# Performance work log

Measured on AMD Instinct MI355X. Metric: run time of the kernel, lower is better.

Reference implementation:

```python
import jax, jax.numpy as jnp
import numpy as np

HIDDEN = 1024
NUM_HEADS = 16
HEAD_SIZE = HIDDEN // NUM_HEADS  # 64
SQ, SK, B = 256, 1024, 8


def setup_inputs() -> dict:
    key = jax.random.key(0)
    ks = jax.random.split(key, 8)
    s = 0.02
    return {
        "x": jax.random.normal(ks[0], (SQ, B, HIDDEN), jnp.float32),
        "memory": jax.random.normal(ks[1], (SK, B, HIDDEN), jnp.float32),
        "Wq": jax.random.normal(ks[2], (HIDDEN, HIDDEN), jnp.float32) * s,
        "bq": jax.random.normal(ks[3], (HIDDEN,), jnp.float32) * s,
        "Wkv": jax.random.normal(ks[4], (2 * HIDDEN, HIDDEN), jnp.float32) * s,
        "bkv": jax.random.normal(ks[5], (2 * HIDDEN,), jnp.float32) * s,
        "Wd": jax.random.normal(ks[6], (HIDDEN, HIDDEN), jnp.float32) * s,
        "bd": jax.random.normal(ks[7], (HIDDEN,), jnp.float32) * s,
    }


def reference(x, memory, Wq, bq, Wkv, bkv, Wd, bd):
    # x: (Sq, B, E), memory: (Sk, B, E)  -- sequence-first layout
    Sq, Bb, E = x.shape
    Sk = memory.shape[0]
    H, Dh = NUM_HEADS, HEAD_SIZE

    q = x @ Wq.T + bq            # (Sq, B, E)
    kv = memory @ Wkv.T + bkv    # (Sk, B, 2E)

    # view (..., H, Dh) then composite permute (1,3,0,2):
    # NOTE: the original module's chained permutes put tensors in
    # (batch, head_size, seq, num_heads) layout, so the score matmul
    # contracts over num_heads and head_size acts as the head axis.
    q = q.reshape(Sq, Bb, H, Dh).transpose((1, 3, 0, 2))          # (B, Dh, Sq, H)
    kv = kv.reshape(Sk, Bb, H, 2 * Dh)
    k = kv[..., :Dh].transpose((1, 3, 0, 2))                       # (B, Dh, Sk, H)
    v = kv[..., Dh:].transpose((1, 3, 0, 2))                       # (B, Dh, Sk, H)

    scale = 1.0 / np.sqrt(float(Dh)).astype(np.float32)
    scores = jnp.einsum('bdqh,bdkh->bdqk', q, k) * scale           # (B, Dh, Sq, Sk)
    attn = jax.nn.softmax(scores, axis=-1)
    # attention_dropout omitted (eval mode / p=0)
    ctx = jnp.einsum('bdqk,bdkh->bdqh', attn, v)                   # (B, Dh, Sq, H)

    # transpose(1,2) -> (B, Sq, Dh, H), reshape concatenates Dh-major
    ctx = ctx.transpose((0, 2, 1, 3)).reshape(Bb, Sq, E)
    ctx = ctx.transpose((1, 0, 2))                                 # (Sq, B, E)
    out = ctx @ Wd.T + bd
    # output dropout omitted (eval mode / p=0)
    return out
```

## Files before the change

### kernel.cpp

```cpp
#include <hip/hip_runtime.h>


typedef float f32x4 __attribute__((ext_vector_type(4)));
typedef __bf16 bf16x8 __attribute__((ext_vector_type(8)));
typedef short s16x8 __attribute__((ext_vector_type(8)));
typedef unsigned int u32x2 __attribute__((ext_vector_type(2)));

__device__ __forceinline__ unsigned short f2bf(float f) {
    unsigned int u = __builtin_bit_cast(unsigned int, f);
    u += 0x7fffu + ((u >> 16) & 1u);
    return (unsigned short)(u >> 16);
}
__device__ __forceinline__ unsigned cvt_pk_bf16(float lo, float hi_) {
    unsigned r;
    asm("v_cvt_pk_bf16_f32 %0, %1, %2" : "=v"(r) : "v"(lo), "v"(hi_));
    return r;
}

__global__ void cvt_f32_bf16(const float* __restrict__ src,
                             unsigned short* __restrict__ dst) {
    int i = (blockIdx.x * 256 + threadIdx.x) * 8;
    float4 a = *reinterpret_cast<const float4*>(src + i);
    float4 b = *reinterpret_cast<const float4*>(src + i + 4);
    s16x8 o;
    o[0] = (short)f2bf(a.x); o[1] = (short)f2bf(a.y);
    o[2] = (short)f2bf(a.z); o[3] = (short)f2bf(a.w);
    o[4] = (short)f2bf(b.x); o[5] = (short)f2bf(b.y);
    o[6] = (short)f2bf(b.z); o[7] = (short)f2bf(b.w);
    *reinterpret_cast<s16x8*>(dst + i) = o;
}

template <int OUT_BF16>
__global__ __launch_bounds__(256, 2)
void gemm_bt(const unsigned short* __restrict__ A,
             const unsigned short* __restrict__ Bw,
             const float* __restrict__ bias,
             void* __restrict__ Cout,
             int M, int N, int K, float scale) {
    __shared__ unsigned short As[128][64];
    __shared__ unsigned short Bs[128][64];

    const int tid = threadIdx.x;
    const int bm = blockIdx.x, bn = blockIdx.y;
    const int lane = tid & 63;
    const int w = tid >> 6;
    const int wr = w >> 1, wc = w & 1;
    const int l15 = lane & 15, lg = lane >> 4;

    f32x4 acc[4][4] = {};

    for (int k0 = 0; k0 < K; k0 += 64) {
#pragma unroll
        for (int it = 0; it < 8; ++it) {
            const int isB = it >> 2;
            int cc = ((it & 3) << 8) + tid;
            int row = cc >> 3, slot = cc & 7;
            const unsigned short* src = isB ? Bw : A;
            int grow = (isB ? bn : bm) * 128 + row;
            s16x8 v = *reinterpret_cast<const s16x8*>(
                src + (size_t)grow * K + k0 + slot * 8);
            unsigned short(*sm)[64] = isB ? Bs : As;
            *reinterpret_cast<s16x8*>(&sm[row][(slot ^ (row & 7)) * 8]) = v;
        }
        __syncthreads();

#pragma unroll
        for (int kk = 0; kk < 2; ++kk) {
            bf16x8 afr[4], bfr[4];
#pragma unroll
            for (int mi = 0; mi < 4; ++mi) {
                int row = wr * 64 + mi * 16 + l15;
                int slot = (kk * 4 + lg) ^ (row & 7);
                afr[mi] = *reinterpret_cast<const bf16x8*>(&As[row][slot * 8]);
            }
#pragma unroll
            for (int nj = 0; nj < 4; ++nj) {
                int row = wc * 64 + nj * 16 + l15;
                int slot = (kk * 4 + lg) ^ (row & 7);
                bfr[nj] = *reinterpret_cast<const bf16x8*>(&Bs[row][slot * 8]);
            }
#pragma unroll
            for (int mi = 0; mi < 4; ++mi)
#pragma unroll
                for (int nj = 0; nj < 4; ++nj)
                    acc[mi][nj] = __builtin_amdgcn_mfma_f32_16x16x32_bf16(
                        afr[mi], bfr[nj], acc[mi][nj], 0, 0, 0);
        }
        __syncthreads();
    }

#pragma unroll
    for (int nj = 0; nj < 4; ++nj) {
        int n = bn * 128 + wc * 64 + nj * 16 + l15;
        float bv = bias[n];
#pragma unroll
        for (int mi = 0; mi < 4; ++mi) {
#pragma unroll
            for (int r = 0; r < 4; ++r) {
                int m = bm * 128 + wr * 64 + mi * 16 + lg * 4 + r;
                float val = (acc[mi][nj][r] + bv) * scale;
                if (OUT_BF16)
                    ((unsigned short*)Cout)[(size_t)m * N + n] = f2bf(val);
                else
                    ((float*)Cout)[(size_t)m * N + n] = val;
            }
        }
    }
}

__global__ __launch_bounds__(256, 2)
void transpose_kv(const unsigned short* __restrict__ kvb,
                  unsigned short* __restrict__ Kp,
                  unsigned short* __restrict__ Vp) {
    __shared__ unsigned short Tl[32 * 1024];
    const int b = blockIdx.x, skc = blockIdx.y, dc = blockIdx.z;
    const int tid = threadIdx.x;
    const int sk0 = skc * 32;
#pragma unroll
    for (int it = 0; it < 16; ++it) {
        int c = it * 256 + tid;
        int r = c >> 7, w = c & 127;
        int seg = w >> 2, j = w & 3;
        int col = (seg >> 1) * 128 + (seg & 1) * 64 + dc * 32 + j * 8;
        s16x8 v = *reinterpret_cast<const s16x8*>(
            kvb + (size_t)((sk0 + r) * 8 + b) * 2048 + col);
        *reinterpret_cast<s16x8*>(&Tl[r * 1024 + seg * 32 + j * 8]) = v;
    }
    __syncthreads();
    const int dl = tid >> 3;
#pragma unroll
    for (int it = 0; it < 8; ++it) {
        int sub = it * 8 + (tid & 7);
        int r = sub >> 1, hh = sub & 1;
        s16x8 o;
#pragma unroll
        for (int e = 0; e < 8; ++e) {
            int h = hh * 8 + e;
            o[e] = Tl[r * 1024 + (h * 2) * 32 + dl];
        }
        *reinterpret_cast<s16x8*>(
            Kp + ((size_t)(b * 64 + dc * 32 + dl) * 1024 + sk0 + r) * 16 + hh * 8) = o;
    }
#pragma unroll
    for (int it = 0; it < 8; ++it) {
        int sub = it * 8 + (tid & 7);
        int h = sub >> 2, oct = sub & 3;
        s16x8 o;
#pragma unroll
        for (int e = 0; e < 8; ++e) {
            int r = oct * 8 + e;
            o[e] = Tl[r * 1024 + (h * 2 + 1) * 32 + dl];
        }
        *reinterpret_cast<s16x8*>(
            Vp + ((size_t)(b * 64 + dc * 32 + dl) * 32 + skc) * 512 + h * 32 + oct * 8) = o;
    }
}

__global__ __launch_bounds__(256, 2)
void transpose_q(const unsigned short* __restrict__ qb,
                 unsigned short* __restrict__ Qp) {
    __shared__ unsigned short Tl[32 * 512];
    const int b = blockIdx.x, sqc = blockIdx.y, dc = blockIdx.z;
    const int tid = threadIdx.x;
    const int sq0 = sqc * 32;
#pragma unroll
    for (int it = 0; it < 8; ++it) {
        int c = it * 256 + tid;
        int r = c >> 6, w = c & 63;
        int h = w >> 2, j = w & 3;
        s16x8 v = *reinterpret_cast<const s16x8*>(
            qb + (size_t)((sq0 + r) * 8 + b) * 1024 + h * 64 + dc * 32 + j * 8);
        *reinterpret_cast<s16x8*>(&Tl[r * 512 + h * 32 + j * 8]) = v;
    }
    __syncthreads();
    const int dl = tid >> 3;
#pragma unroll
    for (int it = 0; it < 8; ++it) {
        int sub = it * 8 + (tid & 7);
        int r = sub >> 1, hh = sub & 1;
        s16x8 o;
#pragma unroll
        for (int e = 0; e < 8; ++e)
            o[e] = Tl[r * 512 + (hh * 8 + e) * 32 + dl];
        *reinterpret_cast<s16x8*>(
            Qp + ((size_t)(b * 64 + dc * 32 + dl) * 256 + sq0 + r) * 16 + hh * 8) = o;
    }
}

__global__ __launch_bounds__(256, 4)
void attn_partial(const unsigned short* __restrict__ Qp,
                  const unsigned short* __restrict__ Kp,
                  const unsigned short* __restrict__ Vp,
                  float* __restrict__ ctxp,
                  float* __restrict__ lp) {
    __shared__ alignas(16) unsigned short KsU[64 * 16];
    __shared__ alignas(16) unsigned short VsU[2 * 512];
    __shared__ alignas(16) unsigned short Plds[4][2][16][40];

    const int bdsp = blockIdx.x;
    const int bd = bdsp >> 1, sp = bdsp & 1;
    const int tid = threadIdx.x;
    const int w = tid >> 6, lane = tid & 63;
    const int l15 = lane & 15, lg = lane >> 4, effLg = lg & 1;

    s16x8 zero8 = {};
    const bf16x8 zfr = __builtin_bit_cast(bf16x8, zero8);

    bf16x8 qfr[4];
#pragma unroll
    for (int st = 0; st < 4; ++st) {
        int sq = w * 64 + st * 16 + l15;
        bf16x8 t = *reinterpret_cast<const bf16x8*>(
            Qp + ((size_t)bd * 256 + sq) * 16 + effLg * 8);
        qfr[st] = (lg < 2) ? t : zfr;
    }

    const int li = tid & 127;
    const bool isV = tid >= 128;
    const unsigned short* src =
        (isV ? Vp : Kp) + (size_t)bd * 16384 + sp * 8192 + li * 8;
    unsigned short* dst = (isV ? VsU : KsU) + li * 8;

    f32x4 ctx[4] = {};
    float lq[4] = {0.f, 0.f, 0.f, 0.f};

    s16x8 pfch = *reinterpret_cast<const s16x8*>(src);

    for (int it = 0; it < 8; ++it) {
        *reinterpret_cast<s16x8*>(dst) = pfch;
        __syncthreads();
        if (it < 7) pfch = *reinterpret_cast<const s16x8*>(src + (it + 1) * 1024);

        bf16x8 kf[4];
#pragma unroll
        for (int t4 = 0; t4 < 4; ++t4) {
            bf16x8 t = *reinterpret_cast<const bf16x8*>(
                KsU + (t4 * 16 + l15) * 16 + effLg * 8);
            kf[t4] = (lg < 2) ? t : zfr;
        }
        bf16x8 vf0 = *reinterpret_cast<const bf16x8*>(VsU + l15 * 32 + lg * 8);
        bf16x8 vf1 = *reinterpret_cast<const bf16x8*>(VsU + 512 + l15 * 32 + lg * 8);

#pragma unroll
        for (int st = 0; st < 4; ++st) {
            f32x4 z = {};
            f32x4 s0 = __builtin_amdgcn_mfma_f32_16x16x32_bf16(kf[0], qfr[st], z, 0, 0, 0);
            f32x4 s1 = __builtin_amdgcn_mfma_f32_16x16x32_bf16(kf[1], qfr[st], z, 0, 0, 0);
            f32x4 s2 = __builtin_amdgcn_mfma_f32_16x16x32_bf16(kf[2], qfr[st], z, 0, 0, 0);
            f32x4 s3 = __builtin_amdgcn_mfma_f32_16x16x32_bf16(kf[3], qfr[st], z, 0, 0, 0);

            float p0[4], p1[4], p2[4], p3[4];
#pragma unroll
            for (int r = 0; r < 4; ++r) {
                p0[r] = __expf(s0[r]); p1[r] = __expf(s1[r]);
                p2[r] = __expf(s2[r]); p3[r] = __expf(s3[r]);
            }
            float ps = ((p0[0] + p0[1]) + (p0[2] + p0[3])) +
                       ((p1[0] + p1[1]) + (p1[2] + p1[3])) +
                       ((p2[0] + p2[1]) + (p2[2] + p2[3])) +
                       ((p3[0] + p3[1]) + (p3[2] + p3[3]));
            ps += __shfl_xor(ps, 16);
            ps += __shfl_xor(ps, 32);
            lq[st] += ps;

            u32x2 wA, wB;
            wA[0] = cvt_pk_bf16(p0[0], p0[1]); wA[1] = cvt_pk_bf16(p0[2], p0[3]);
            wB[0] = cvt_pk_bf16(p1[0], p1[1]); wB[1] = cvt_pk_bf16(p1[2], p1[3]);
            *reinterpret_cast<u32x2*>(&Plds[w][0][l15][lg * 4]) = wA;
            *reinterpret_cast<u32x2*>(&Plds[w][0][l15][16 + lg * 4]) = wB;
            u32x2 wC, wD;
            wC[0] = cvt_pk_bf16(p2[0], p2[1]); wC[1] = cvt_pk_bf16(p2[2], p2[3]);
            wD[0] = cvt_pk_bf16(p3[0], p3[1]); wD[1] = cvt_pk_bf16(p3[2], p3[3]);
            *reinterpret_cast<u32x2*>(&Plds[w][1][l15][lg * 4]) = wC;
            *reinterpret_cast<u32x2*>(&Plds[w][1][l15][16 + lg * 4]) = wD;

            bf16x8 pfr0 = *reinterpret_cast<const bf16x8*>(&Plds[w][0][l15][lg * 8]);
            ctx[st] = __builtin_amdgcn_mfma_f32_16x16x32_bf16(pfr0, vf0, ctx[st], 0, 0, 0);
            bf16x8 pfr1 = *reinterpret_cast<const bf16x8*>(&Plds[w][1][l15][lg * 8]);
            ctx[st] = __builtin_amdgcn_mfma_f32_16x16x32_bf16(pfr1, vf1, ctx[st], 0, 0, 0);
        }
        __syncthreads();
    }

#pragma unroll
    for (int st = 0; st < 4; ++st) {
        if (lg == 0)
            lp[(size_t)bdsp * 256 + w * 64 + st * 16 + l15] = lq[st];
#pragma unroll
        for (int r = 0; r < 4; ++r) {
            int sq = w * 64 + st * 16 + lg * 4 + r;
            ctxp[((size_t)bdsp * 256 + sq) * 16 + l15] = ctx[st][r];
        }
    }
}

__global__ __launch_bounds__(256, 8)
void attn_combine(const float* __restrict__ ctxp,
                  const float* __restrict__ lp,
                  unsigned short* __restrict__ ctxb) {
    int idx = blockIdx.x * 256 + threadIdx.x;
    int bd = idx >> 8, sq = idx & 255;
    int b = bd >> 6, d = bd & 63;
    const float* c0 = ctxp + ((size_t)(bd * 2) * 256 + sq) * 16;
    const float* c1 = c0 + 256 * 16;
    float inv = 1.f / (lp[(size_t)(bd * 2) * 256 + sq] +
                       lp[(size_t)(bd * 2 + 1) * 256 + sq]);
    s16x8 o0, o1;
#pragma unroll
    for (int j = 0; j < 2; ++j) {
        float4 a0 = *reinterpret_cast<const float4*>(c0 + j * 8);
        float4 a1 = *reinterpret_cast<const float4*>(c0 + j * 8 + 4);
        float4 b0 = *reinterpret_cast<const float4*>(c1 + j * 8);
        float4 b1 = *reinterpret_cast<const float4*>(c1 + j * 8 + 4);
        s16x8& o = j ? o1 : o0;
        o[0] = (short)f2bf((a0.x + b0.x) * inv);
        o[1] = (short)f2bf((a0.y + b0.y) * inv);
        o[2] = (short)f2bf((a0.z + b0.z) * inv);
        o[3] = (short)f2bf((a0.w + b0.w) * inv);
        o[4] = (short)f2bf((a1.x + b1.x) * inv);
        o[5] = (short)f2bf((a1.y + b1.y) * inv);
        o[6] = (short)f2bf((a1.z + b1.z) * inv);
        o[7] = (short)f2bf((a1.w + b1.w) * inv);
    }
    unsigned short* dst = ctxb + (size_t)(sq * 8 + b) * 1024 + d * 16;
    *reinterpret_cast<s16x8*>(dst) = o0;
    *reinterpret_cast<s16x8*>(dst + 8) = o1;
}

extern "C" void kernel_launch(void* const* d_in, const int* in_sizes, int n_in,
                              void* d_out, int out_size, void* d_ws, size_t ws_size,
                              hipStream_t stream) {
    const float* x   = (const float*)d_in[0];
    const float* mem = (const float*)d_in[1];
    const float* Wq  = (const float*)d_in[2];
    const float* bq  = (const float*)d_in[3];
    const float* Wkv = (const float*)d_in[4];
    const float* bkv = (const float*)d_in[5];
    const float* Wd  = (const float*)d_in[6];
    const float* bd  = (const float*)d_in[7];
    float* out = (float*)d_out;

    const size_t M = 1024 * 1024;
    unsigned short* ws    = (unsigned short*)d_ws;
    unsigned short* qbuf  = ws;
    unsigned short* kvbuf = ws + 2 * M;
    unsigned short* Kp    = ws + 18 * M;
    unsigned short* Vp    = ws + 26 * M;
    unsigned short* xb    = ws + 18 * M;
    unsigned short* mb    = ws + 20 * M;
    unsigned short* wqb   = ws + 28 * M;
    unsigned short* wkvb  = ws + 29 * M;
    unsigned short* ctxb  = ws + 2 * M;
    unsigned short* Qp    = ws + 4 * M;
    unsigned short* wdb   = ws + 6 * M;
    float*          ctxp  = (float*)(ws + 8 * M);
    float*          lp    = (float*)(ws + 17 * M);

    cvt_f32_bf16<<<(2048 * 1024) / 2048, 256, 0, stream>>>(x, xb);
    cvt_f32_bf16<<<(8192 * 1024) / 2048, 256, 0, stream>>>(mem, mb);
    cvt_f32_bf16<<<(1024 * 1024) / 2048, 256, 0, stream>>>(Wq, wqb);
    cvt_f32_bf16<<<(2048 * 1024) / 2048, 256, 0, stream>>>(Wkv, wkvb);

    gemm_bt<1><<<dim3(2048 / 128, 1024 / 128), 256, 0, stream>>>(
        xb, wqb, bq, qbuf, 2048, 1024, 1024, 0.125f);
    gemm_bt<1><<<dim3(8192 / 128, 2048 / 128), 256, 0, stream>>>(
        mb, wkvb, bkv, kvbuf, 8192, 2048, 1024, 1.0f);

    transpose_kv<<<dim3(8, 32, 2), 256, 0, stream>>>(kvbuf, Kp, Vp);
    transpose_q<<<dim3(8, 8, 2), 256, 0, stream>>>(qbuf, Qp);

    cvt_f32_bf16<<<(1024 * 1024) / 2048, 256, 0, stream>>>(Wd, wdb);

    attn_partial<<<1024, 256, 0, stream>>>(Qp, Kp, Vp, ctxp, lp);
    attn_combine<<<512, 256, 0, stream>>>(ctxp, lp, ctxb);

    gemm_bt<0><<<dim3(2048 / 128, 1024 / 128), 256, 0, stream>>>(
        ctxb, wdb, bd, out, 2048, 1024, 1024, 1.0f);
}
```

Measured before the change: 170.8 us.

## Load GEMM tiles via direct global-to-LDS and fuse input conversions

The GEMM tile loads now use global_load_lds, which writes global memory straight into LDS and skips the register round trip. The swizzle moves to the global address side so the LDS layout stays the same. The four fp32-to-bf16 conversion launches become one fused kernel, cutting launch overhead. Both conversion paths now use the packed hardware bf16 convert instruction instead of manual rounding.

```diff
diff --git a/kernel.cpp b/kernel.cpp
--- a/kernel.cpp
+++ b/kernel.cpp
@@ -5,6 +5,7 @@
 typedef __bf16 bf16x8 __attribute__((ext_vector_type(8)));
 typedef short s16x8 __attribute__((ext_vector_type(8)));
 typedef unsigned int u32x2 __attribute__((ext_vector_type(2)));
+typedef unsigned int u32x4 __attribute__((ext_vector_type(4)));
 
 __device__ __forceinline__ unsigned short f2bf(float f) {
     unsigned int u = __builtin_bit_cast(unsigned int, f);
@@ -15,6 +16,18 @@
     unsigned r;
     asm("v_cvt_pk_bf16_f32 %0, %1, %2" : "=v"(r) : "v"(lo), "v"(hi_));
     return r;
+}
+__device__ __forceinline__ s16x8 cvt8(float4 a, float4 b) {
+    u32x4 r;
+    r[0] = cvt_pk_bf16(a.x, a.y); r[1] = cvt_pk_bf16(a.z, a.w);
+    r[2] = cvt_pk_bf16(b.x, b.y); r[3] = cvt_pk_bf16(b.z, b.w);
+    return __builtin_bit_cast(s16x8, r);
+}
+__device__ __forceinline__ void gload_lds16(const unsigned short* g,
+                                            unsigned short* l) {
+    __builtin_amdgcn_global_load_lds(
+        (const __attribute__((address_space(1))) void*)g,
+        (__attribute__((address_space(3))) void*)l, 16, 0, 0);
 }
 
 __global__ void cvt_f32_bf16(const float* __restrict__ src,
@@ -22,12 +35,27 @@
     int i = (blockIdx.x * 256 + threadIdx.x) * 8;
     float4 a = *reinterpret_cast<const float4*>(src + i);
     float4 b = *reinterpret_cast<const float4*>(src + i + 4);
-    s16x8 o;
-    o[0] = (short)f2bf(a.x); o[1] = (short)f2bf(a.y);
-    o[2] = (short)f2bf(a.z); o[3] = (short)f2bf(a.w);
-    o[4] = (short)f2bf(b.x); o[5] = (short)f2bf(b.y);
-    o[6] = (short)f2bf(b.z); o[7] = (short)f2bf(b.w);
-    *reinterpret_cast<s16x8*>(dst + i) = o;
+    *reinterpret_cast<s16x8*>(dst + i) = cvt8(a, b);
+}
+
+__global__ void cvt_fused4(const float* __restrict__ x,
+                           const float* __restrict__ mem,
+                           const float* __restrict__ wq,
+                           const float* __restrict__ wkv,
+                           unsigned short* __restrict__ xb,
+                           unsigned short* __restrict__ mb,
+                           unsigned short* __restrict__ wqb,
+                           unsigned short* __restrict__ wkvb) {
+    long t = (long)blockIdx.x * 256 + threadIdx.x;
+    const float* src; unsigned short* dst; long off;
+    if (t < 262144)                { src = x;   dst = xb;   off = t; }
+    else if (t < 262144 + 1048576) { src = mem; dst = mb;   off = t - 262144; }
+    else if (t < 1441792)          { src = wq;  dst = wqb;  off = t - 1310720; }
+    else                           { src = wkv; dst = wkvb; off = t - 1441792; }
+    long i = off * 8;
+    float4 a = *reinterpret_cast<const float4*>(src + i);
+    float4 b = *reinterpret_cast<const float4*>(src + i + 4);
+    *reinterpret_cast<s16x8*>(dst + i) = cvt8(a, b);
 }
 
 template <int OUT_BF16>
@@ -53,14 +81,15 @@
 #pragma unroll
         for (int it = 0; it < 8; ++it) {
             const int isB = it >> 2;
-            int cc = ((it & 3) << 8) + tid;
-            int row = cc >> 3, slot = cc & 7;
+            int cbase = ((it & 3) << 8) + w * 64;
+            int c = cbase + lane;
+            int row = c >> 3, slotp = c & 7;
+            int slot = slotp ^ (row & 7);
             const unsigned short* src = isB ? Bw : A;
             int grow = (isB ? bn : bm) * 128 + row;
-            s16x8 v = *reinterpret_cast<const s16x8*>(
-                src + (size_t)grow * K + k0 + slot * 8);
-            unsigned short(*sm)[64] = isB ? Bs : As;
-            *reinterpret_cast<s16x8*>(&sm[row][(slot ^ (row & 7)) * 8]) = v;
+            const unsigned short* gptr = src + (size_t)grow * K + k0 + slot * 8;
+            unsigned short* lptr = (isB ? &Bs[0][0] : &As[0][0]) + cbase * 8;
+            gload_lds16(gptr, lptr);
         }
         __syncthreads();
 
@@ -356,10 +385,7 @@
     float*          ctxp  = (float*)(ws + 8 * M);
     float*          lp    = (float*)(ws + 17 * M);
 
-    cvt_f32_bf16<<<(2048 * 1024) / 2048, 256, 0, stream>>>(x, xb);
-    cvt_f32_bf16<<<(8192 * 1024) / 2048, 256, 0, stream>>>(mem, mb);
-    cvt_f32_bf16<<<(1024 * 1024) / 2048, 256, 0, stream>>>(Wq, wqb);
-    cvt_f32_bf16<<<(2048 * 1024) / 2048, 256, 0, stream>>>(Wkv, wkvb);
+    cvt_fused4<<<6656, 256, 0, stream>>>(x, mem, Wq, Wkv, xb, mb, wqb, wkvb);
 
     gemm_bt<1><<<dim3(2048 / 128, 1024 / 128), 256, 0, stream>>>(
         xb, wqb, bq, qbuf, 2048, 1024, 1024, 0.125f);
@@ -369,7 +395,7 @@
     transpose_kv<<<dim3(8, 32, 2), 256, 0, stream>>>(kvbuf, Kp, Vp);
     transpose_q<<<dim3(8, 8, 2), 256, 0, stream>>>(qbuf, Qp);
 
-    cvt_f32_bf16<<<(1024 * 1024) / 2048, 256, 0, stream>>>(Wd, wdb);
+    cvt_f32_bf16<<<512, 256, 0, stream>>>(Wd, wdb);
 
     attn_partial<<<1024, 256, 0, stream>>>(Qp, Kp, Vp, ctxp, lp);
     attn_combine<<<512, 256, 0, stream>>>(ctxp, lp, ctxb);
```

Result: faster. 150.1 us (-12.1%).
